# Performance work log

Measured on AMD Instinct MI355X. Metric: run time of the kernel, lower is better.

Reference implementation:

```python
import jax, jax.numpy as jnp
import numpy as np
from jax.ops import segment_sum

N_NODES = 100000
N_EDGES = 1600000
N_GRAPHS = 128
HIDDEN = 128
N_CLASSES = 10


def setup_inputs() -> dict:
    key = jax.random.key(0)
    ks = jax.random.split(key, 8)
    src = jax.random.randint(ks[0], (N_EDGES,), 0, N_NODES, dtype=jnp.int32)
    dst = jax.random.randint(ks[1], (N_EDGES,), 0, N_NODES, dtype=jnp.int32)
    graph_ids = jnp.sort(jax.random.randint(ks[2], (N_NODES,), 0, N_GRAPHS, dtype=jnp.int32))
    W1 = jax.random.normal(ks[3], (1, HIDDEN), dtype=jnp.float32)
    b1 = jnp.zeros((HIDDEN,), jnp.float32)
    W2 = jax.random.normal(ks[4], (HIDDEN, HIDDEN), dtype=jnp.float32) * 0.05
    b2 = jnp.zeros((HIDDEN,), jnp.float32)
    Wc = jax.random.normal(ks[5], (HIDDEN, N_CLASSES), dtype=jnp.float32) * 0.05
    bc = jnp.zeros((N_CLASSES,), jnp.float32)
    return {"src": src, "dst": dst, "graph_ids": graph_ids,
            "W1": W1, "b1": b1, "W2": W2, "b2": b2, "Wc": Wc, "bc": bc}


def _graph_conv(h, src, dst, norm_src, norm_dst, W, b, n_nodes):
    # DGL GraphConv, norm='both': D_out^{-1/2} gather -> scatter-sum -> W -> D_in^{-1/2} -> +b
    hs = h * norm_src[:, None]
    agg = segment_sum(hs[src], dst, num_segments=n_nodes)  # [N, F_in]
    return agg @ W * norm_dst[:, None] + b


def reference(src, dst, graph_ids, W1, b1, W2, b2, Wc, bc):
    n_nodes = graph_ids.shape[0]
    ones_e = jnp.ones(src.shape[0], jnp.float32)
    indeg = segment_sum(ones_e, dst, num_segments=n_nodes)
    outdeg = segment_sum(ones_e, src, num_segments=n_nodes)
    norm_src = jnp.clip(outdeg, 1.0, None) ** -0.5
    norm_dst = jnp.clip(indeg, 1.0, None) ** -0.5

    h = indeg[:, None]  # node feature = in-degree, [N, 1]
    h = jax.nn.relu(_graph_conv(h, src, dst, norm_src, norm_dst, W1, b1, n_nodes))
    h = jax.nn.relu(_graph_conv(h, src, dst, norm_src, norm_dst, W2, b2, n_nodes))

    # dgl.mean_nodes: per-graph mean pooling
    sums = segment_sum(h, graph_ids, num_segments=N_GRAPHS)          # [G, H]
    cnts = segment_sum(jnp.ones(n_nodes, jnp.float32), graph_ids, num_segments=N_GRAPHS)
    hg = sums / jnp.clip(cnts, 1.0, None)[:, None]
    return hg @ Wc + bc  # [G, n_classes]
```

## Files before the change

kernel.cpp:

```cpp
#include <hip/hip_runtime.h>

#define N_NODES   100000
#define N_EDGES   1600000
#define N_GRAPHS  128
#define HIDDEN    128
#define N_CLASSES 10

#define BSH   9
#define BSZ   512
#define NBUCK 196
#define CAP   16384
#define PCH   4096
#define PTH   512

typedef unsigned int   uint;
typedef unsigned short ushort;
typedef unsigned char  uchar;

__global__ __launch_bounds__(PTH)
void k_part(const int* __restrict__ src, const int* __restrict__ dst,
            unsigned* __restrict__ bcur1, unsigned* __restrict__ bcur2,
            unsigned* __restrict__ tmp1, ushort* __restrict__ tmp2, int nE) {
    __shared__ unsigned hist[256], scanT[256], lcur[256], base[256];
    __shared__ unsigned stag4[PCH];
    __shared__ uchar    stagB[PCH];
    int t = threadIdx.x;
    int e0 = blockIdx.x * PCH;
    int e1 = min(e0 + PCH, nE);
    int cntE = e1 - e0;

    if (t < 256) hist[t] = 0;
    __syncthreads();
    for (int e = e0 + t; e < e1; e += PTH)
        atomicAdd(&hist[dst[e] >> BSH], 1u);
    __syncthreads();
    unsigned v = (t < 256) ? hist[t] : 0u;
    if (t < 256) scanT[t] = v;
    __syncthreads();
    for (int off = 1; off < 256; off <<= 1) {
        unsigned add = (t < 256 && t >= off) ? scanT[t - off] : 0u;
        __syncthreads();
        if (t < 256) scanT[t] += add;
        __syncthreads();
    }
    if (t < 256) {
        unsigned excl = scanT[t] - v;
        lcur[t] = excl;
        if (v > 0) { unsigned g = atomicAdd(&bcur1[t], v); base[t] = (unsigned)t * CAP + g - excl; }
    }
    __syncthreads();
    for (int e = e0 + t; e < e1; e += PTH) {
        int d = dst[e], s = src[e];
        int b = d >> BSH;
        unsigned p = atomicAdd(&lcur[b], 1u);
        stag4[p] = ((unsigned)(d & (BSZ - 1)) << 17) | (unsigned)s;
        stagB[p] = (uchar)b;
    }
    __syncthreads();
    for (int i = t; i < cntE; i += PTH) {
        unsigned b = stagB[i];
        unsigned a = base[b] + (unsigned)i;
        if (a < (b + 1u) * CAP) tmp1[a] = stag4[i];
    }
    __syncthreads();

    if (t < 256) hist[t] = 0;
    __syncthreads();
    for (int e = e0 + t; e < e1; e += PTH)
        atomicAdd(&hist[src[e] >> BSH], 1u);
    __syncthreads();
    v = (t < 256) ? hist[t] : 0u;
    if (t < 256) scanT[t] = v;
    __syncthreads();
    for (int off = 1; off < 256; off <<= 1) {
        unsigned add = (t < 256 && t >= off) ? scanT[t - off] : 0u;
        __syncthreads();
        if (t < 256) scanT[t] += add;
        __syncthreads();
    }
    if (t < 256) {
        unsigned excl = scanT[t] - v;
        lcur[t] = excl;
        if (v > 0) { unsigned g = atomicAdd(&bcur2[t], v); base[t] = (unsigned)t * CAP + g - excl; }
    }
    __syncthreads();
    ushort* st2 = (ushort*)stag4;
    for (int e = e0 + t; e < e1; e += PTH) {
        int s = src[e];
        int b = s >> BSH;
        unsigned p = atomicAdd(&lcur[b], 1u);
        st2[p]   = (ushort)(s & (BSZ - 1));
        stagB[p] = (uchar)b;
    }
    __syncthreads();
    for (int i = t; i < cntE; i += PTH) {
        unsigned b = stagB[i];
        unsigned a = base[b] + (unsigned)i;
        if (a < (b + 1u) * CAP) tmp2[a] = st2[i];
    }
}

__global__ __launch_bounds__(1024)
void k_ind_csr(const unsigned* __restrict__ bcur1, const unsigned* __restrict__ tmp1,
               const unsigned* __restrict__ bcur2, const ushort* __restrict__ tmp2,
               unsigned* __restrict__ indeg, float* __restrict__ ns,
               float* __restrict__ hs0, int* __restrict__ rs,
               int* __restrict__ csr) {
    __shared__ unsigned cin[BSZ], cout[BSZ], pref[BSZ], lcur[BSZ];
    int b = blockIdx.x, t = threadIdx.x;
    if (t < BSZ) { cin[t] = 0; cout[t] = 0; }
    __syncthreads();
    unsigned f1 = min(bcur1[b], (unsigned)CAP);
    const unsigned* tp1 = tmp1 + (size_t)b * CAP;
    for (unsigned i = t; i < f1; i += 1024) atomicAdd(&cin[tp1[i] >> 17], 1u);
    unsigned f2 = min(bcur2[b], (unsigned)CAP);
    const ushort* tp2 = tmp2 + (size_t)b * CAP;
    for (unsigned i = t; i < f2; i += 1024) atomicAdd(&cout[tp2[i]], 1u);
    __syncthreads();
    unsigned v = (t < BSZ) ? cin[t] : 0u;
    if (t < BSZ) pref[t] = v;
    __syncthreads();
    for (int off = 1; off < BSZ; off <<= 1) {
        unsigned add = (t < BSZ && t >= off) ? pref[t - off] : 0u;
        __syncthreads();
        if (t < BSZ) pref[t] += add;
        __syncthreads();
    }
    if (t < BSZ) {
        unsigned excl = pref[t] - v;
        lcur[t] = excl;
        int n = b * BSZ + t;
        if (n < N_NODES) {
            unsigned ci = cin[t], co = cout[t];
            float nsv = rsqrtf(fmaxf((float)co, 1.0f));
            indeg[n] = ci;
            ns[n]    = nsv;
            hs0[n]   = (float)ci * nsv;
            rs[n]    = (int)(b * CAP + excl);
        }
    }
    __syncthreads();
    int* cb = csr + (size_t)b * CAP;
    for (unsigned i = t; i < f1; i += 1024) {
        unsigned e = tp1[i];
        unsigned pos = atomicAdd(&lcur[e >> 17], 1u);
        cb[pos] = (int)(e & 0x1FFFFu);
    }
}

__global__ __launch_bounds__(256)
void k_conv1_info(const int* __restrict__ rs, const int* __restrict__ csr,
                  const float* __restrict__ hs0, const unsigned* __restrict__ indeg,
                  const float* __restrict__ ns,
                  const float* __restrict__ W1, const float* __restrict__ b1,
                  const float* __restrict__ W2,
                  float* __restrict__ U, float* __restrict__ V,
                  float4* __restrict__ info, int nN) {
    __shared__ float sts[128];
    int t = threadIdx.x;
    if (t < 128) {
        float w = W1[t], bb = b1[t];
        sts[t] = (w != 0.0f) ? (-bb / w) : 1e30f;
    }
    __syncthreads();
    for (int k = 2; k <= 128; k <<= 1) {
        for (int j = k >> 1; j > 0; j >>= 1) {
            if (t < 128) {
                int ixj = t ^ j;
                if (ixj > t) {
                    float a = sts[t], bb = sts[ixj];
                    bool up = ((t & k) == 0);
                    if (up ? (a > bb) : (a < bb)) { sts[t] = bb; sts[ixj] = a; }
                }
            }
            __syncthreads();
        }
    }
    if (blockIdx.x < 129 && t < 128) {
        int sg = blockIdx.x;
        float a_rep;
        if (sg == 0)        a_rep = sts[0]   - 1.0f;
        else if (sg == 128) a_rep = sts[127] + 1.0f;
        else                a_rep = 0.5f * (sts[sg - 1] + sts[sg]);
        float u = 0.0f, vv = 0.0f;
        for (int j = 0; j < 128; ++j) {
            float w = W1[j], bb = b1[j];
            if (a_rep * w + bb > 0.0f) {
                float w2 = W2[j * HIDDEN + t];
                u  += w * w2;
                vv += bb * w2;
            }
        }
        U[sg * HIDDEN + t] = u;
        V[sg * HIDDEN + t] = vv;
    }
    int n = blockIdx.x * 256 + t;
    if (n >= nN) return;
    int r0 = rs[n];
    int c  = (int)indeg[n];
    float a = 0.0f;
    #pragma unroll 4
    for (int k = 0; k < c; ++k) a += hs0[csr[r0 + k]];
    float nd = rsqrtf(fmaxf((float)c, 1.0f));
    a *= nd;
    float nsv = ns[n];
    int sg = 0;
    #pragma unroll
    for (int j = 0; j < 128; ++j) sg += (sts[j] < a) ? 1 : 0;
    info[n] = make_float4(nsv * a, nsv, __int_as_float(sg), nd);
}

__global__ __launch_bounds__(256)
void k_conv2_pool(const int* __restrict__ rs, const int* __restrict__ csr,
                  const float4* __restrict__ info, const unsigned* __restrict__ indeg,
                  const float* __restrict__ U, const float* __restrict__ V,
                  const int* __restrict__ graph_ids, const float* __restrict__ b2,
                  float* __restrict__ pool, float* __restrict__ cnt, int nN) {
    __shared__ float sA[256], sB[256], sND[256];
    __shared__ int   sSg[256], sGr[256], sR[256], sC[256];
    int blockBase = blockIdx.x * 256;
    int t = threadIdx.x;
    int n = blockBase + t;

    if (n < nN) {
        int r0 = rs[n], c = (int)indeg[n];
        float A = 0.0f, B = 0.0f;
        int mn = 255, mx = 0;
        #pragma unroll 4
        for (int k = 0; k < c; ++k) {
            float4 nf = info[csr[r0 + k]];
            int sg = __float_as_int(nf.z);
            A += nf.x; B += nf.y;
            mn = min(mn, sg); mx = max(mx, sg);
        }
        sA[t] = A; sB[t] = B;
        sSg[t] = (mn << 8) | mx;
        sR[t] = r0; sC[t] = c;
        sND[t] = info[n].w;
        sGr[t] = graph_ids[n];
    }
    __syncthreads();

    int w = t >> 6, lane = t & 63;
    int n0 = blockBase + 64 * w;
    if (n0 >= nN) return;
    int n1 = min(n0 + 64, nN);

    float bb0 = b2[lane], bb1 = b2[64 + lane];
    int gcur = -1;
    float racc0 = 0.0f, racc1 = 0.0f, cl = 0.0f;

    for (int node = n0; node < n1; ++node) {
        int i = node - blockBase;
        int pk = sSg[i], mn = pk >> 8, mx = pk & 255;
        float acc0, acc1;
        if (mn >= mx) {
            int sg = min(mn, 128);
            float A = sA[i], B = sB[i];
            const float* Ur = U + sg * HIDDEN;
            const float* Vr = V + sg * HIDDEN;
            acc0 = A * Ur[lane]      + B * Vr[lane];
            acc1 = A * Ur[64 + lane] + B * Vr[64 + lane];
        } else {
            acc0 = 0.0f; acc1 = 0.0f;
            int r0 = sR[i], c = sC[i];
            for (int k = 0; k < c; ++k) {
                float4 nf = info[csr[r0 + k]];
                int sg = __float_as_int(nf.z);
                const float* Ur = U + sg * HIDDEN;
                const float* Vr = V + sg * HIDDEN;
                acc0 += nf.x * Ur[lane]      + nf.y * Vr[lane];
                acc1 += nf.x * Ur[64 + lane] + nf.y * Vr[64 + lane];
            }
        }
        float nd = sND[i];
        float r0v = fmaxf(nd * acc0 + bb0, 0.0f);
        float r1v = fmaxf(nd * acc1 + bb1, 0.0f);
        int g = sGr[i];
        if (g != gcur) {
            if (gcur >= 0) {
                atomicAdd(&pool[gcur * HIDDEN + lane],      racc0);
                atomicAdd(&pool[gcur * HIDDEN + 64 + lane], racc1);
                if (lane == 0) atomicAdd(&cnt[gcur], cl);
            }
            gcur = g; racc0 = 0.0f; racc1 = 0.0f; cl = 0.0f;
        }
        racc0 += r0v; racc1 += r1v; cl += 1.0f;
    }
    if (gcur >= 0) {
        atomicAdd(&pool[gcur * HIDDEN + lane],      racc0);
        atomicAdd(&pool[gcur * HIDDEN + 64 + lane], racc1);
        if (lane == 0) atomicAdd(&cnt[gcur], cl);
    }
}

__global__ void k_final(const float* __restrict__ pool, const float* __restrict__ cnt,
                        const float* __restrict__ Wc, const float* __restrict__ bc,
                        float* __restrict__ out) {
    int t = blockIdx.x * blockDim.x + threadIdx.x;
    if (t >= N_GRAPHS * N_CLASSES) return;
    int g = t / N_CLASSES, c = t % N_CLASSES;
    float inv = 1.0f / fmaxf(cnt[g], 1.0f);
    float acc = bc[c];
    for (int j = 0; j < HIDDEN; ++j)
        acc += pool[g * HIDDEN + j] * inv * Wc[j * N_CLASSES + c];
    out[t] = acc;
}

extern "C" void kernel_launch(void* const* d_in, const int* in_sizes, int n_in,
                              void* d_out, int out_size, void* d_ws, size_t ws_size,
                              hipStream_t stream) {
    const int*   src       = (const int*)d_in[0];
    const int*   dst       = (const int*)d_in[1];
    const int*   graph_ids = (const int*)d_in[2];
    const float* W1        = (const float*)d_in[3];
    const float* b1        = (const float*)d_in[4];
    const float* W2        = (const float*)d_in[5];
    const float* b2        = (const float*)d_in[6];
    const float* Wc        = (const float*)d_in[7];
    const float* bc        = (const float*)d_in[8];
    float* out = (float*)d_out;

    char* ws = (char*)d_ws;
    size_t off = 0;
    auto alloc = [&](size_t elems) { void* p = ws + off; off += elems * 4; return p; };

    unsigned* bcur1 = (unsigned*)alloc(256);
    unsigned* bcur2 = (unsigned*)alloc(256);
    float*    pool  = (float*)   alloc(N_GRAPHS * HIDDEN);
    float*    cnt   = (float*)   alloc(N_GRAPHS);
    size_t zero_bytes = off;
    float4*   info  = (float4*)  alloc((size_t)N_NODES * 4);
    unsigned* tmp1  = (unsigned*)alloc((size_t)NBUCK * CAP);
    ushort*   tmp2  = (ushort*)  alloc((size_t)NBUCK * CAP / 2);
    int*      csr   = (int*)     alloc((size_t)NBUCK * CAP);
    int*      rs    = (int*)     alloc(N_NODES);
    unsigned* indeg = (unsigned*)alloc(N_NODES);
    float*    nsA   = (float*)   alloc(N_NODES);
    float*    hs0   = (float*)   alloc(N_NODES);
    float*    U     = (float*)   alloc(129 * HIDDEN);
    float*    V     = (float*)   alloc(129 * HIDDEN);

    hipMemsetAsync(d_ws, 0, zero_bytes, stream);

    int pblocks = (N_EDGES + PCH - 1) / PCH;
    int nblocks = (N_NODES + 255) / 256;
    k_part      <<<pblocks, PTH, 0, stream>>>(src, dst, bcur1, bcur2, tmp1, tmp2, N_EDGES);
    k_ind_csr   <<<NBUCK, 1024, 0, stream>>>(bcur1, tmp1, bcur2, tmp2, indeg, nsA, hs0, rs, csr);
    k_conv1_info<<<nblocks, 256, 0, stream>>>(rs, csr, hs0, indeg, nsA, W1, b1, W2, U, V, info, N_NODES);
    k_conv2_pool<<<nblocks, 256, 0, stream>>>(rs, csr, info, indeg, U, V, graph_ids, b2, pool, cnt, N_NODES);
    k_final     <<<(N_GRAPHS * N_CLASSES + 255) / 256, 256, 0, stream>>>(pool, cnt, Wc, bc, out);
}
```

Before: 182.9 us.

## Cache edge indices in registers and split node gathers across multiple lanes

The partition kernel now loads src/dst once into registers and reuses them across both histogram and scatter passes, where before it re-read them from global memory. The conv1 gather gives each node two lanes and the conv2 gather gives each node four lanes, combined with shuffle reductions, which shortens the serial per-node degree loop. Grids grow to match. In conv2 only one wavefront of each block then runs the 64-node dense phase, so per-block parallelism in that phase drops. The conv1 threshold count is also split across the lane pair.

After: 183.2 us. Within noise of the previous version (+0.2%).

```diff
diff --git a/kernel.cpp b/kernel.cpp
--- a/kernel.cpp
+++ b/kernel.cpp
@@ -12,6 +12,7 @@
 #define CAP   16384
 #define PCH   4096
 #define PTH   512
+#define PIT   (PCH / PTH)
 
 typedef unsigned int   uint;
 typedef unsigned short ushort;
@@ -29,10 +30,17 @@
     int e1 = min(e0 + PCH, nE);
     int cntE = e1 - e0;
 
+    int sv[PIT], dv[PIT];
     if (t < 256) hist[t] = 0;
     __syncthreads();
-    for (int e = e0 + t; e < e1; e += PTH)
-        atomicAdd(&hist[dst[e] >> BSH], 1u);
+    #pragma unroll
+    for (int m = 0; m < PIT; ++m) {
+        int e = e0 + t + m * PTH;
+        if (e < e1) {
+            sv[m] = src[e]; dv[m] = dst[e];
+            atomicAdd(&hist[dv[m] >> BSH], 1u);
+        }
+    }
     __syncthreads();
     unsigned v = (t < 256) ? hist[t] : 0u;
     if (t < 256) scanT[t] = v;
@@ -49,12 +57,16 @@
         if (v > 0) { unsigned g = atomicAdd(&bcur1[t], v); base[t] = (unsigned)t * CAP + g - excl; }
     }
     __syncthreads();
-    for (int e = e0 + t; e < e1; e += PTH) {
-        int d = dst[e], s = src[e];
-        int b = d >> BSH;
-        unsigned p = atomicAdd(&lcur[b], 1u);
-        stag4[p] = ((unsigned)(d & (BSZ - 1)) << 17) | (unsigned)s;
-        stagB[p] = (uchar)b;
+    #pragma unroll
+    for (int m = 0; m < PIT; ++m) {
+        int e = e0 + t + m * PTH;
+        if (e < e1) {
+            int d = dv[m], s = sv[m];
+            int b = d >> BSH;
+            unsigned p = atomicAdd(&lcur[b], 1u);
+            stag4[p] = ((unsigned)(d & (BSZ - 1)) << 17) | (unsigned)s;
+            stagB[p] = (uchar)b;
+        }
     }
     __syncthreads();
     for (int i = t; i < cntE; i += PTH) {
@@ -66,8 +78,11 @@
 
     if (t < 256) hist[t] = 0;
     __syncthreads();
-    for (int e = e0 + t; e < e1; e += PTH)
-        atomicAdd(&hist[src[e] >> BSH], 1u);
+    #pragma unroll
+    for (int m = 0; m < PIT; ++m) {
+        int e = e0 + t + m * PTH;
+        if (e < e1) atomicAdd(&hist[sv[m] >> BSH], 1u);
+    }
     __syncthreads();
     v = (t < 256) ? hist[t] : 0u;
     if (t < 256) scanT[t] = v;
@@ -85,12 +100,16 @@
     }
     __syncthreads();
     ushort* st2 = (ushort*)stag4;
-    for (int e = e0 + t; e < e1; e += PTH) {
-        int s = src[e];
-        int b = s >> BSH;
-        unsigned p = atomicAdd(&lcur[b], 1u);
-        st2[p]   = (ushort)(s & (BSZ - 1));
-        stagB[p] = (uchar)b;
+    #pragma unroll
+    for (int m = 0; m < PIT; ++m) {
+        int e = e0 + t + m * PTH;
+        if (e < e1) {
+            int s = sv[m];
+            int b = s >> BSH;
+            unsigned p = atomicAdd(&lcur[b], 1u);
+            st2[p]   = (ushort)(s & (BSZ - 1));
+            stagB[p] = (uchar)b;
+        }
     }
     __syncthreads();
     for (int i = t; i < cntE; i += PTH) {
@@ -194,20 +213,25 @@
         U[sg * HIDDEN + t] = u;
         V[sg * HIDDEN + t] = vv;
     }
-    int n = blockIdx.x * 256 + t;
-    if (n >= nN) return;
-    int r0 = rs[n];
-    int c  = (int)indeg[n];
+    int node = blockIdx.x * 128 + (t >> 1);
+    if (node >= nN) return;
+    int j  = t & 1;
+    int r0 = rs[node];
+    int c  = (int)indeg[node];
     float a = 0.0f;
     #pragma unroll 4
-    for (int k = 0; k < c; ++k) a += hs0[csr[r0 + k]];
+    for (int k = j; k < c; k += 2) a += hs0[csr[r0 + k]];
+    a += __shfl_xor(a, 1);
     float nd = rsqrtf(fmaxf((float)c, 1.0f));
-    a *= nd;
-    float nsv = ns[n];
-    int sg = 0;
-    #pragma unroll
-    for (int j = 0; j < 128; ++j) sg += (sts[j] < a) ? 1 : 0;
-    info[n] = make_float4(nsv * a, nsv, __int_as_float(sg), nd);
+    float av = a * nd;
+    int sgp = 0;
+    #pragma unroll
+    for (int q = 0; q < 64; ++q) sgp += (sts[2 * q + j] < av) ? 1 : 0;
+    sgp += __shfl_xor(sgp, 1);
+    if (j == 0) {
+        float nsv = ns[node];
+        info[node] = make_float4(nsv * av, nsv, __int_as_float(sgp), nd);
+    }
 }
 
 __global__ __launch_bounds__(256)
@@ -216,56 +240,63 @@
                   const float* __restrict__ U, const float* __restrict__ V,
                   const int* __restrict__ graph_ids, const float* __restrict__ b2,
                   float* __restrict__ pool, float* __restrict__ cnt, int nN) {
-    __shared__ float sA[256], sB[256], sND[256];
-    __shared__ int   sSg[256], sGr[256], sR[256], sC[256];
-    int blockBase = blockIdx.x * 256;
+    __shared__ float sA[64], sB[64], sND[64];
+    __shared__ int   sSg[64], sGr[64], sR[64], sC[64];
+    int blockBase = blockIdx.x * 64;
     int t = threadIdx.x;
-    int n = blockBase + t;
-
-    if (n < nN) {
-        int r0 = rs[n], c = (int)indeg[n];
-        float A = 0.0f, B = 0.0f;
-        int mn = 255, mx = 0;
+    int node = blockBase + (t >> 2);
+    int j = t & 3;
+
+    float A = 0.0f, B = 0.0f;
+    int mn = 255, mx = 0;
+    int r0 = 0, c = 0;
+    if (node < nN) {
+        r0 = rs[node]; c = (int)indeg[node];
         #pragma unroll 4
-        for (int k = 0; k < c; ++k) {
+        for (int k = j; k < c; k += 4) {
             float4 nf = info[csr[r0 + k]];
             int sg = __float_as_int(nf.z);
             A += nf.x; B += nf.y;
             mn = min(mn, sg); mx = max(mx, sg);
         }
-        sA[t] = A; sB[t] = B;
-        sSg[t] = (mn << 8) | mx;
-        sR[t] = r0; sC[t] = c;
-        sND[t] = info[n].w;
-        sGr[t] = graph_ids[n];
-    }
-    __syncthreads();
-
-    int w = t >> 6, lane = t & 63;
-    int n0 = blockBase + 64 * w;
-    if (n0 >= nN) return;
-    int n1 = min(n0 + 64, nN);
+    }
+    A += __shfl_xor(A, 1); A += __shfl_xor(A, 2);
+    B += __shfl_xor(B, 1); B += __shfl_xor(B, 2);
+    mn = min(mn, __shfl_xor(mn, 1)); mn = min(mn, __shfl_xor(mn, 2));
+    mx = max(mx, __shfl_xor(mx, 1)); mx = max(mx, __shfl_xor(mx, 2));
+    if (node < nN && j == 0) {
+        int i = t >> 2;
+        sA[i] = A; sB[i] = B;
+        sSg[i] = (mn << 8) | mx;
+        sR[i] = r0; sC[i] = c;
+        sND[i] = info[node].w;
+        sGr[i] = graph_ids[node];
+    }
+    __syncthreads();
+    if (t >= 64) return;
+    int lane = t;
 
     float bb0 = b2[lane], bb1 = b2[64 + lane];
     int gcur = -1;
     float racc0 = 0.0f, racc1 = 0.0f, cl = 0.0f;
 
-    for (int node = n0; node < n1; ++node) {
-        int i = node - blockBase;
-        int pk = sSg[i], mn = pk >> 8, mx = pk & 255;
+    for (int i = 0; i < 64; ++i) {
+        int n = blockBase + i;
+        if (n >= nN) break;
+        int pk = sSg[i], smn = pk >> 8, smx = pk & 255;
         float acc0, acc1;
-        if (mn >= mx) {
-            int sg = min(mn, 128);
-            float A = sA[i], B = sB[i];
+        if (smn >= smx) {
+            int sg = min(smn, 128);
+            float Av = sA[i], Bv = sB[i];
             const float* Ur = U + sg * HIDDEN;
             const float* Vr = V + sg * HIDDEN;
-            acc0 = A * Ur[lane]      + B * Vr[lane];
-            acc1 = A * Ur[64 + lane] + B * Vr[64 + lane];
+            acc0 = Av * Ur[lane]      + Bv * Vr[lane];
+            acc1 = Av * Ur[64 + lane] + Bv * Vr[64 + lane];
         } else {
             acc0 = 0.0f; acc1 = 0.0f;
-            int r0 = sR[i], c = sC[i];
-            for (int k = 0; k < c; ++k) {
-                float4 nf = info[csr[r0 + k]];
+            int rr = sR[i], cc = sC[i];
+            for (int k = 0; k < cc; ++k) {
+                float4 nf = info[csr[rr + k]];
                 int sg = __float_as_int(nf.z);
                 const float* Ur = U + sg * HIDDEN;
                 const float* Vr = V + sg * HIDDEN;
@@ -343,11 +374,12 @@
 
     hipMemsetAsync(d_ws, 0, zero_bytes, stream);
 
-    int pblocks = (N_EDGES + PCH - 1) / PCH;
-    int nblocks = (N_NODES + 255) / 256;
+    int pblocks  = (N_EDGES + PCH - 1) / PCH;
+    int c1blocks = (N_NODES + 127) / 128;
+    int c2blocks = (N_NODES + 63) / 64;
     k_part      <<<pblocks, PTH, 0, stream>>>(src, dst, bcur1, bcur2, tmp1, tmp2, N_EDGES);
     k_ind_csr   <<<NBUCK, 1024, 0, stream>>>(bcur1, tmp1, bcur2, tmp2, indeg, nsA, hs0, rs, csr);
-    k_conv1_info<<<nblocks, 256, 0, stream>>>(rs, csr, hs0, indeg, nsA, W1, b1, W2, U, V, info, N_NODES);
-    k_conv2_pool<<<nblocks, 256, 0, stream>>>(rs, csr, info, indeg, U, V, graph_ids, b2, pool, cnt, N_NODES);
+    k_conv1_info<<<c1blocks, 256, 0, stream>>>(rs, csr, hs0, indeg, nsA, W1, b1, W2, U, V, info, N_NODES);
+    k_conv2_pool<<<c2blocks, 256, 0, stream>>>(rs, csr, info, indeg, U, V, graph_ids, b2, pool, cnt, N_NODES);
     k_final     <<<(N_GRAPHS * N_CLASSES + 255) / 256, 256, 0, stream>>>(pool, cnt, Wc, bc, out);
 }
```
